# Kernel tuning notes

Measured on AMD Instinct MI355X. Metric: run time of the kernel, lower is better.

Reference implementation:

```python
import jax, jax.numpy as jnp
import numpy as np

WEIGHT = 1e-7       # lambda for the CRF loss
SIGMA_RGB = 15.0    # color-similarity bandwidth
SIGMA_XY = 100.0    # spatial-proximity bandwidth
SCALE = 0.5         # scale_factor (sigma_xy is multiplied by it in forward)


def setup_inputs() -> dict:
    key = jax.random.key(0)
    k1, k2 = jax.random.split(key)
    images = jax.random.uniform(k1, (4, 3, 128, 128), jnp.float32) * 255.0  # [0,255] RGB
    logits = jax.random.normal(k2, (4, 4, 128, 128), jnp.float32)
    segmentations = jax.nn.softmax(logits, axis=1)  # softmaxed logits, N*K*H*W
    return {"images": images, "segmentations": segmentations}


def _crf_loss(images, segmentations):
    n, k, h, w = segmentations.shape
    # F.interpolate(images, scale_factor=0.5, mode='nearest') == stride-2 subsample
    img_s = images[:, :, ::2, ::2]
    # F.interpolate(segs, scale_factor=0.5, mode='bilinear', align_corners=False)
    # for exact /2 downscale == 2x2 average pooling
    hs, ws = h // 2, w // 2
    seg_s = segmentations.reshape(n, k, hs, 2, ws, 2).mean(axis=(3, 5))  # [n,k,hs,ws]

    P = hs * ws
    yy, xx = jnp.meshgrid(jnp.arange(hs, dtype=jnp.float32),
                          jnp.arange(ws, dtype=jnp.float32), indexing='ij')
    sigma_xy_eff = SIGMA_XY * SCALE
    pos = jnp.stack([xx, yy], axis=-1).reshape(P, 2) / sigma_xy_eff      # [P,2]
    rgb = img_s.reshape(n, 3, P).transpose(0, 2, 1) / SIGMA_RGB          # [n,P,3]
    feats = jnp.concatenate([jnp.broadcast_to(pos[None], (n, P, 2)), rgb], axis=-1)  # [n,P,5]

    # exact dense Gaussian bilateral kernel W_ij = exp(-0.5*||f_i - f_j||^2)
    sq = jnp.sum(feats * feats, axis=-1)                                 # [n,P]
    d2 = sq[:, :, None] + sq[:, None, :] - 2.0 * jnp.einsum('npc,nqc->npq', feats, feats)
    Wk = jnp.exp(-0.5 * jnp.maximum(d2, 0.0))                            # [n,P,P]

    S = seg_s.reshape(n, k, P)
    AS = jnp.einsum('npq,nkq->nkp', Wk, S)                               # bilateral-filtered segs
    loss = -jnp.sum(S * AS) / jnp.float32(n)
    return (WEIGHT * loss).reshape(1)


def reference(images, segmentations):
    return _crf_loss(images, segmentations)
```

## Files before the change

### kernel.cpp

```cpp
#include <hip/hip_runtime.h>

#define NB   4
#define KCH  4
#define P    4096
#define REC  12
#define QT   64
#define BLK  256
#define PT   4

#if __has_builtin(__builtin_amdgcn_exp2f)
#define EXPFN(x) __builtin_amdgcn_exp2f(x)
#define FSCALE 1.2011224087864498f
#else
#define EXPFN(x) __expf(x)
#define FSCALE 1.0f
#endif

__global__ __launch_bounds__(64) void crf_prep(const float* __restrict__ images,
                                               const float* __restrict__ segs,
                                               float* __restrict__ rec,
                                               float* __restrict__ out) {
    int idx = blockIdx.x * 64 + threadIdx.x;
    if (idx == 0) out[0] = 0.0f;
    int n = idx >> 12;
    int p = idx & (P - 1);
    int i = p >> 6;
    int j = p & 63;
    const float* img = images + (size_t)n * 3 * 16384;
    int rowoff = 256 * i;
    float2 ir = ((const float2*)(img + 0 * 16384 + rowoff))[j];
    float2 ig = ((const float2*)(img + 1 * 16384 + rowoff))[j];
    float2 ib = ((const float2*)(img + 2 * 16384 + rowoff))[j];
    float x = (float)j * (FSCALE / 50.0f);
    float y = (float)i * (FSCALE / 50.0f);
    float r = ir.x * (FSCALE / 15.0f);
    float g = ig.x * (FSCALE / 15.0f);
    float b = ib.x * (FSCALE / 15.0f);
    float h = -0.5f * (x * x + y * y + r * r + g * g + b * b);
    float* o = rec + (size_t)idx * REC;
    o[0] = x; o[1] = y; o[2] = r; o[3] = g; o[4] = b; o[5] = h;
    const float* sg = segs + (size_t)n * KCH * 16384;
#pragma unroll
    for (int k = 0; k < KCH; ++k) {
        float2 s0 = ((const float2*)(sg + k * 16384 + rowoff))[j];
        float2 s1 = ((const float2*)(sg + k * 16384 + rowoff + 128))[j];
        o[6 + k] = 0.25f * ((s0.x + s0.y) + (s1.x + s1.y));
    }
    o[10] = 0.0f; o[11] = 0.0f;
}

__global__ __launch_bounds__(256) void crf_main(const float* __restrict__ rec,
                                                float* __restrict__ out) {
    __shared__ float lds[QT * REC];
    __shared__ float wsum[BLK / 64];

    int t = threadIdx.x;
    int pb = blockIdx.x;
    int n = pb >> 2;
    int pbase = (pb & 3) * (BLK * PT);
    int qbase = blockIdx.y * QT;
    const float* base = rec + (size_t)n * P * REC;

    const float4* src4 = (const float4*)(base + (size_t)qbase * REC);
    float4* lds4 = (float4*)lds;
    if (t < QT * REC / 4) lds4[t] = src4[t];

    float rp[PT][10];
#pragma unroll
    for (int pi = 0; pi < PT; ++pi) {
        const float* r0 = base + (size_t)(pbase + t + pi * BLK) * REC;
        float4 a = ((const float4*)r0)[0];
        float4 b = ((const float4*)r0)[1];
        float2 c = ((const float2*)r0)[4];
        rp[pi][0] = a.x; rp[pi][1] = a.y; rp[pi][2] = a.z; rp[pi][3] = a.w;
        rp[pi][4] = b.x; rp[pi][5] = b.y; rp[pi][6] = b.z; rp[pi][7] = b.w;
        rp[pi][8] = c.x; rp[pi][9] = c.y;
    }
    __syncthreads();

    float acc[PT] = {0.f, 0.f, 0.f, 0.f};
#pragma unroll 2
    for (int q = 0; q < QT; ++q) {
        const float4* rq = (const float4*)(lds + q * REC);
        float4 f0 = rq[0];
        float4 f1 = rq[1];
        float4 f2 = rq[2];
#pragma unroll
        for (int pi = 0; pi < PT; ++pi) {
            float d = rp[pi][5] + f1.y;
            d = fmaf(rp[pi][0], f0.x, d);
            d = fmaf(rp[pi][1], f0.y, d);
            d = fmaf(rp[pi][2], f0.z, d);
            d = fmaf(rp[pi][3], f0.w, d);
            d = fmaf(rp[pi][4], f1.x, d);
            float w = EXPFN(d);
            float sd = rp[pi][6] * f1.z;
            sd = fmaf(rp[pi][7], f1.w, sd);
            sd = fmaf(rp[pi][8], f2.x, sd);
            sd = fmaf(rp[pi][9], f2.y, sd);
            acc[pi] = fmaf(w, sd, acc[pi]);
        }
    }

    float acc_all = (acc[0] + acc[1]) + (acc[2] + acc[3]);
#pragma unroll
    for (int off = 32; off > 0; off >>= 1)
        acc_all += __shfl_down(acc_all, off, 64);
    if ((t & 63) == 0) wsum[t >> 6] = acc_all;
    __syncthreads();
    if (t == 0) {
        float s = (wsum[0] + wsum[1]) + (wsum[2] + wsum[3]);
        atomicAdd(out, s * (-2.5e-8f));
    }
}

extern "C" void kernel_launch(void* const* d_in, const int* in_sizes, int n_in,
                              void* d_out, int out_size, void* d_ws, size_t ws_size,
                              hipStream_t stream) {
    const float* images = (const float*)d_in[0];
    const float* segs   = (const float*)d_in[1];
    float* out = (float*)d_out;
    float* rec = (float*)d_ws;

    crf_prep<<<dim3(256), dim3(64), 0, stream>>>(images, segs, rec, out);
    crf_main<<<dim3(16, 64), dim3(256), 0, stream>>>(rec, out);
}
```

Before: 79.98 us.

## Exploit kernel symmetry to compute only upper-triangular pair tiles

After: 78.07 us. 2.4% less time.

```diff
diff --git a/kernel.cpp b/kernel.cpp
--- a/kernel.cpp
+++ b/kernel.cpp
@@ -6,7 +6,9 @@
 #define REC  12
 #define QT   64
 #define BLK  256
-#define PT   4
+#define PT   2
+#define NPT  8
+#define NBLK 288
 
 #if __has_builtin(__builtin_amdgcn_exp2f)
 #define EXPFN(x) __builtin_amdgcn_exp2f(x)
@@ -55,10 +57,18 @@
     __shared__ float wsum[BLK / 64];
 
     int t = threadIdx.x;
-    int pb = blockIdx.x;
-    int n = pb >> 2;
-    int pbase = (pb & 3) * (BLK * PT);
-    int qbase = blockIdx.y * QT;
+    int n = blockIdx.y;
+
+    static const int cum[NPT] = {0, 64, 120, 168, 208, 240, 264, 280};
+    int b = blockIdx.x;
+    int pt = 0;
+#pragma unroll
+    for (int i = 1; i < NPT; ++i) pt += (b >= cum[i]) ? 1 : 0;
+    int qc = b - cum[pt] + 8 * pt;
+    int pbase = pt * (BLK * PT);
+    int qbase = qc * QT;
+    bool mixed = (qc >> 3) == pt;
+
     const float* base = rec + (size_t)n * P * REC;
 
     const float4* src4 = (const float4*)(base + (size_t)qbase * REC);
@@ -70,39 +80,70 @@
     for (int pi = 0; pi < PT; ++pi) {
         const float* r0 = base + (size_t)(pbase + t + pi * BLK) * REC;
         float4 a = ((const float4*)r0)[0];
-        float4 b = ((const float4*)r0)[1];
+        float4 b4 = ((const float4*)r0)[1];
         float2 c = ((const float2*)r0)[4];
         rp[pi][0] = a.x; rp[pi][1] = a.y; rp[pi][2] = a.z; rp[pi][3] = a.w;
-        rp[pi][4] = b.x; rp[pi][5] = b.y; rp[pi][6] = b.z; rp[pi][7] = b.w;
+        rp[pi][4] = b4.x; rp[pi][5] = b4.y; rp[pi][6] = b4.z; rp[pi][7] = b4.w;
         rp[pi][8] = c.x; rp[pi][9] = c.y;
     }
     __syncthreads();
 
-    float acc[PT] = {0.f, 0.f, 0.f, 0.f};
-#pragma unroll 2
-    for (int q = 0; q < QT; ++q) {
-        const float4* rq = (const float4*)(lds + q * REC);
-        float4 f0 = rq[0];
-        float4 f1 = rq[1];
-        float4 f2 = rq[2];
+    float acc[PT] = {0.f, 0.f};
+    float acc_all;
+
+    if (!mixed) {
+#pragma unroll 4
+        for (int q = 0; q < QT; ++q) {
+            const float4* rq = (const float4*)(lds + q * REC);
+            float4 f0 = rq[0];
+            float4 f1 = rq[1];
+            float4 f2 = rq[2];
 #pragma unroll
-        for (int pi = 0; pi < PT; ++pi) {
-            float d = rp[pi][5] + f1.y;
-            d = fmaf(rp[pi][0], f0.x, d);
-            d = fmaf(rp[pi][1], f0.y, d);
-            d = fmaf(rp[pi][2], f0.z, d);
-            d = fmaf(rp[pi][3], f0.w, d);
-            d = fmaf(rp[pi][4], f1.x, d);
-            float w = EXPFN(d);
-            float sd = rp[pi][6] * f1.z;
-            sd = fmaf(rp[pi][7], f1.w, sd);
-            sd = fmaf(rp[pi][8], f2.x, sd);
-            sd = fmaf(rp[pi][9], f2.y, sd);
-            acc[pi] = fmaf(w, sd, acc[pi]);
+            for (int pi = 0; pi < PT; ++pi) {
+                float d = rp[pi][5] + f1.y;
+                d = fmaf(rp[pi][0], f0.x, d);
+                d = fmaf(rp[pi][1], f0.y, d);
+                d = fmaf(rp[pi][2], f0.z, d);
+                d = fmaf(rp[pi][3], f0.w, d);
+                d = fmaf(rp[pi][4], f1.x, d);
+                float w = EXPFN(d);
+                float sd = rp[pi][6] * f1.z;
+                sd = fmaf(rp[pi][7], f1.w, sd);
+                sd = fmaf(rp[pi][8], f2.x, sd);
+                sd = fmaf(rp[pi][9], f2.y, sd);
+                acc[pi] = fmaf(w, sd, acc[pi]);
+            }
         }
+        acc_all = 2.0f * (acc[0] + acc[1]);
+    } else {
+#pragma unroll 4
+        for (int q = 0; q < QT; ++q) {
+            const float4* rq = (const float4*)(lds + q * REC);
+            float4 f0 = rq[0];
+            float4 f1 = rq[1];
+            float4 f2 = rq[2];
+            int qg = qbase + q;
+#pragma unroll
+            for (int pi = 0; pi < PT; ++pi) {
+                int pg = pbase + t + pi * BLK;
+                float d = rp[pi][5] + f1.y;
+                d = fmaf(rp[pi][0], f0.x, d);
+                d = fmaf(rp[pi][1], f0.y, d);
+                d = fmaf(rp[pi][2], f0.z, d);
+                d = fmaf(rp[pi][3], f0.w, d);
+                d = fmaf(rp[pi][4], f1.x, d);
+                float w = EXPFN(d);
+                float sd = rp[pi][6] * f1.z;
+                sd = fmaf(rp[pi][7], f1.w, sd);
+                sd = fmaf(rp[pi][8], f2.x, sd);
+                sd = fmaf(rp[pi][9], f2.y, sd);
+                float f = (qg > pg) ? 2.0f : ((qg == pg) ? 1.0f : 0.0f);
+                acc[pi] = fmaf(w, sd * f, acc[pi]);
+            }
+        }
+        acc_all = acc[0] + acc[1];
     }
 
-    float acc_all = (acc[0] + acc[1]) + (acc[2] + acc[3]);
 #pragma unroll
     for (int off = 32; off > 0; off >>= 1)
         acc_all += __shfl_down(acc_all, off, 64);
@@ -123,5 +164,5 @@
     float* rec = (float*)d_ws;
 
     crf_prep<<<dim3(256), dim3(64), 0, stream>>>(images, segs, rec, out);
-    crf_main<<<dim3(16, 64), dim3(256), 0, stream>>>(rec, out);
+    crf_main<<<dim3(NBLK, NB), dim3(256), 0, stream>>>(rec, out);
 }
```
